# Optimization experiments

Hardware: AMD Instinct MI355X
Metric: run time of the kernel (lower is better)

Reference implementation:

```python
import jax, jax.numpy as jnp
from jax import lax
import numpy as np

B, C, H, W, K = 8, 256, 128, 128, 4


def setup_inputs() -> dict:
    key = jax.random.key(0)
    ks = jax.random.split(key, 21)
    s = 0.05
    return {
        'frm_feat': jax.random.normal(ks[0], (B, C, H, W), jnp.float32),
        'other_feat': jax.random.normal(ks[1], (B, C, H, W), jnp.float32),
        'conv3x3_w': jax.random.normal(ks[2], (C, 2 * C, 3, 3), jnp.float32) * (1.0 / np.sqrt(2 * C * 9).astype(np.float32)),
        'conv3x3_b': jax.random.normal(ks[3], (C,), jnp.float32) * s,
        'a1_w': jax.random.normal(ks[4], (C, 2), jnp.float32) * s,
        'a1_b': jax.random.normal(ks[5], (C,), jnp.float32) * s,
        'a2_w': jax.random.normal(ks[6], (C, 2), jnp.float32) * s,
        'a2_b': jax.random.normal(ks[7], (C,), jnp.float32) * s,
        'a3_w': jax.random.normal(ks[8], (C, 2), jnp.float32) * s,
        'a3_b': jax.random.normal(ks[9], (C,), jnp.float32) * s,
        'ug_w': jax.random.normal(ks[10], (K, C), jnp.float32) * (1.0 / np.sqrt(C).astype(np.float32)),
        'ug_b': jax.random.normal(ks[11], (K,), jnp.float32) * s,
        'recon_w': jax.random.normal(ks[12], (C, C), jnp.float32) * (1.0 / np.sqrt(C).astype(np.float32)),
        'recon_b': jax.random.normal(ks[13], (C,), jnp.float32) * s,
        'sp_w': jax.random.normal(ks[14], (), jnp.float32),
        'sp_b': jax.random.normal(ks[15], (), jnp.float32) * s,
        'spa_w': jax.random.normal(ks[16], (C, C), jnp.float32) * (1.0 / np.sqrt(C).astype(np.float32)),
        'spa_b': jax.random.normal(ks[17], (C,), jnp.float32) * s,
        'spm_w': jax.random.normal(ks[18], (C, C), jnp.float32) * (1.0 / np.sqrt(C).astype(np.float32)),
        'spm_b': jax.random.normal(ks[19], (C,), jnp.float32) * s,
        'alpha': jnp.float32(0.5),
    }


def _make_U(mode, aw, ab, ug_w, ug_b):
    # mode: [B, N, M] -> U: [B, N, K] (softmax over rank K)
    avg = jnp.mean(mode, axis=2)           # [B, N]
    mx = jnp.max(mode, axis=2)             # [B, N]
    feat = jnp.stack([avg, mx], axis=1)    # [B, 2, N]
    feat = jnp.einsum('co,bon->bcn', aw, feat) + ab[None, :, None]  # adapter 1x1 conv: [B, C, N]
    logits = jnp.einsum('kc,bcn->bnk', ug_w, feat) + ug_b           # U_gen 1x1 conv: [B, N, K]
    return jax.nn.softmax(logits, axis=-1)


def reference(frm_feat, other_feat, conv3x3_w, conv3x3_b, a1_w, a1_b, a2_w, a2_b,
              a3_w, a3_b, ug_w, ug_b, recon_w, recon_b, sp_w, sp_b,
              spa_w, spa_b, spm_w, spm_b, alpha):
    b, c, h, w = frm_feat.shape
    x = jnp.concatenate([frm_feat, other_feat], axis=1)  # [B, 2C, H, W]
    Fm = lax.conv_general_dilated(x, conv3x3_w, (1, 1), 'SAME',
                                  dimension_numbers=('NCHW', 'OIHW', 'NCHW'))
    Fm = Fm + conv3x3_b[None, :, None, None]
    Fm = jnp.where(Fm >= 0, Fm, 0.01 * Fm)  # LeakyReLU(0.01)

    # Three mode unfoldings (same math as torch permute/reshape chains)
    mode1 = Fm.reshape(b, c, h * w)                     # [B, C, HW]
    mode2 = jnp.transpose(Fm, (0, 3, 1, 2)).reshape(b, w, c * h)  # [B, W, CH]
    mode3 = jnp.transpose(Fm, (0, 2, 1, 3)).reshape(b, h, c * w)  # [B, H, CW]

    U1 = _make_U(mode1, a1_w, a1_b, ug_w, ug_b)  # [B, C, K]
    U2 = _make_U(mode2, a2_w, a2_b, ug_w, ug_b)  # [B, W, K]
    U3 = _make_U(mode3, a3_w, a3_b, ug_w, ug_b)  # [B, H, K]

    # CP outer-product reconstruction summed over rank, already in [B,C,H,W] layout
    cp = jnp.einsum('bck,bwk,bhk->bchw', U1, U2, U3)
    cp = jnp.einsum('oc,bchw->bohw', recon_w, cp) + recon_b[None, :, None, None]

    # spatial attention: sigmoid(1x1 conv on U3 @ U2^T)
    spatial_att = jax.nn.sigmoid(sp_w * jnp.einsum('bhk,bwk->bhw', U3, U2)[:, None] + sp_b)  # [B,1,H,W]

    # spectral attention
    U23 = jnp.concatenate([U2, U3], axis=1)              # [B, W+H, K]
    F_spe = jnp.einsum('bck,bnk->bcn', U1, U23)          # [B, C, W+H]
    g_avg = jnp.mean(F_spe, axis=-1)                     # [B, C]
    g_max = jnp.max(F_spe, axis=-1)                      # [B, C]
    spec = jax.nn.sigmoid(g_avg @ spa_w.T + spa_b + g_max @ spm_w.T + spm_b)
    spec = jax.nn.sigmoid(spec)[:, :, None, None]        # double sigmoid as in source, [B,C,1,1]

    Watt = spec * spatial_att                            # [B, C, H, W]
    fused = alpha * Watt * frm_feat + (1.0 - alpha) * (1.0 - Watt) * other_feat
    return fused, cp
```

## Files before the change

### kernel.cpp

```cpp
#include <hip/hip_runtime.h>
#include <math.h>

#define BB 8
#define CC 256
#define HH 128
#define WW 128
#define CP_OFF 33554432

#define ZB_OFF   0
#define P1S_OFF  256
#define P1M_OFF  262400
#define P2S_OFF  524544
#define P2M_OFF  525568
#define P3S_OFF  526592
#define P3M_OFF  527616
#define U2_OFF   528640
#define U3_OFF   532736
#define V1_OFF   536832
#define SPEC_OFF 545024
#define WS_ZERO_BYTES (528640 * 4)

typedef __attribute__((ext_vector_type(8))) short bf16x8;
typedef __attribute__((ext_vector_type(4))) float f32x4;

static __device__ __forceinline__ unsigned short f2bf(float f) {
    unsigned u = __float_as_uint(f);
    unsigned r = u + 0x7FFFu + ((u >> 16) & 1u);
    return (unsigned short)(r >> 16);
}
static __device__ __forceinline__ unsigned fkey(float f) {
    unsigned u = __float_as_uint(f);
    return (u & 0x80000000u) ? ~u : (u | 0x80000000u);
}
static __device__ __forceinline__ float fkeydec(unsigned k) {
    return __uint_as_float((k & 0x80000000u) ? (k & 0x7FFFFFFFu) : ~k);
}
static __device__ __forceinline__ void gl_lds16(const void* g, void* l) {
    typedef const __attribute__((address_space(1))) unsigned int* gas_t;
    typedef __attribute__((address_space(3))) unsigned int* las_t;
    gas_t gp = (gas_t)(uintptr_t)g;
    las_t lp = (las_t)(unsigned int)(uintptr_t)l;
    __builtin_amdgcn_global_load_lds(gp, lp, 16, 0, 0);
}

__global__ __launch_bounds__(256) void wt_kernel(
    const float* __restrict__ cw, unsigned short* __restrict__ WtF)
{
    const int g = blockIdx.x * 256 + threadIdx.x;
    const int co = g >> 9, ci = g & 511;
    const int fg = co >> 4, l15c = co & 15;
    const int cic = ci >> 5, l4c = (ci >> 3) & 3, e = ci & 7;
    const int lane = l4c * 16 + l15c;
    const float* s = cw + (size_t)g * 9;
    #pragma unroll
    for (int kh = 0; kh < 3; kh++)
        #pragma unroll
        for (int kw = 0; kw < 3; kw++) {
            const size_t dst =
                ((((size_t)(kh * 16 + cic) * 3 + kw) * 16 + fg) * 64 + lane) * 8 + e;
            WtF[dst] = f2bf(s[kh * 3 + kw]);
        }
}

__global__ __launch_bounds__(256) void xt_kernel(
    const float* __restrict__ frm, const float* __restrict__ oth,
    unsigned short* __restrict__ Xt)
{
    const int w = threadIdx.x & 127, half = threadIdx.x >> 7;
    const int h = blockIdx.x, b = blockIdx.y;
    const float* src = half ? oth : frm;
    const size_t inbase = (((size_t)b * 256) << 14) + ((size_t)h << 7) + w;
    unsigned short* op = Xt + ((((size_t)(b * 128 + h) * 128) + w) << 9) + half * 256;
    #pragma unroll 2
    for (int c8 = 0; c8 < 32; c8++) {
        unsigned short u[8];
        #pragma unroll
        for (int j = 0; j < 8; j++)
            u[j] = f2bf(src[inbase + (((size_t)(c8 * 8 + j)) << 14)]);
        uint4 pk;
        pk.x = (unsigned)u[0] | ((unsigned)u[1] << 16);
        pk.y = (unsigned)u[2] | ((unsigned)u[3] << 16);
        pk.z = (unsigned)u[4] | ((unsigned)u[5] << 16);
        pk.w = (unsigned)u[6] | ((unsigned)u[7] << 16);
        *(uint4*)(op + c8 * 8) = pk;
    }
}

__global__ __launch_bounds__(256, 2) void conv_mfma(
    const unsigned short* __restrict__ WtF,
    const unsigned short* __restrict__ Xt,
    const float* __restrict__ cb,
    const unsigned short* __restrict__ zb,
    float* __restrict__ p1s, unsigned* __restrict__ p1m,
    float* __restrict__ p2s, unsigned* __restrict__ p2m,
    float* __restrict__ p3s, unsigned* __restrict__ p3m)
{
    __shared__ __align__(16) unsigned short lB[2][544 * 8];

    const int tid = threadIdx.x;
    const int swz = (blockIdx.x & 7) * 256 + (blockIdx.x >> 3);
    const int b = swz >> 8;
    const int h = (swz >> 1) & 127;
    const int cohalf = swz & 1;

    const int lane = tid & 63, wid = tid >> 6;
    const int wm = wid & 1, wn = wid >> 1;
    const int l15 = lane & 15, l4 = lane >> 4;
    const int fgBase = cohalf * 8 + wm * 4;

    const unsigned short* baseB[3];
    bool okB[3];
    int dstB[3];
    #pragma unroll
    for (int j = 0; j < 3; j++) {
        const int wi = j * 64 + lane;
        const int wg = wi - 1;
        okB[j] = (wg >= 0) && (wg < WW);
        baseB[j] = Xt + (size_t)b * 8388608
                      + (size_t)(okB[j] ? wg : 0) * 512 + wid * 8;
        dstB[j] = (wid * 136 + j * 64) * 8;
    }
    const unsigned short* baseA = WtF + (size_t)fgBase * 512 + (size_t)lane * 8;

    f32x4 acc[4][4];
    #pragma unroll
    for (int m = 0; m < 4; m++)
        #pragma unroll
        for (int n = 0; n < 4; n++)
            acc[m][n] = (f32x4){0.f, 0.f, 0.f, 0.f};

    auto stageB = [&](int q, int bufi) {
        const int kh = q >> 4;
        const int ci0 = (q & 15) << 5;
        const int hr = h + kh - 1;
        const bool hv = (hr >= 0) && (hr < HH);
        const int boff = (hv ? hr : 0) * 65536 + ci0;
        #pragma unroll
        for (int j = 0; j < 2; j++) {
            const unsigned short* s = (hv && okB[j]) ? (baseB[j] + boff) : zb;
            gl_lds16(s, &lB[bufi][dstB[j]]);
        }
        {
            const unsigned short* s = (hv && okB[2]) ? (baseB[2] + boff) : zb;
            if (lane < 8) gl_lds16(s, &lB[bufi][dstB[2]]);
        }
    };

    auto loadA = [&](int q, bf16x8 (&r)[12]) {
        const unsigned short* p = baseA + (size_t)q * 24576;
        #pragma unroll
        for (int kw = 0; kw < 3; kw++)
            #pragma unroll
            for (int m = 0; m < 4; m++)
                r[kw * 4 + m] = *(const bf16x8*)(p + kw * 8192 + m * 512);
    };

    auto compute = [&](const unsigned short* Bl, bf16x8 (&rA)[12]) {
        #pragma unroll
        for (int kw = 0; kw < 3; kw++) {
            bf16x8 bfr[4];
            #pragma unroll
            for (int n = 0; n < 4; n++) {
                const int unit = l4 * 136 + wn * 64 + n * 16 + l15 + kw;
                bfr[n] = *(const bf16x8*)&Bl[unit * 8];
            }
            #pragma unroll
            for (int m = 0; m < 4; m++)
                #pragma unroll
                for (int n = 0; n < 4; n++)
                    acc[m][n] = __builtin_amdgcn_mfma_f32_16x16x32_bf16(
                        rA[kw * 4 + m], bfr[n], acc[m][n], 0, 0, 0);
        }
    };

    bf16x8 rA0[12], rA1[12];

    stageB(0, 0);
    loadA(0, rA0);

    #pragma unroll 1
    for (int q = 0; q < 46; q += 2) {
        stageB(q + 1, 1);
        loadA(q + 1, rA1);
        __builtin_amdgcn_sched_barrier(0);
        asm volatile("s_waitcnt vmcnt(15)" ::: "memory");
        __builtin_amdgcn_s_barrier();
        __builtin_amdgcn_sched_barrier(0);
        __builtin_amdgcn_s_setprio(1);
        compute(lB[0], rA0);
        __builtin_amdgcn_s_setprio(0);
        __builtin_amdgcn_sched_barrier(0);
        __builtin_amdgcn_s_barrier();

        stageB(q + 2, 0);
        loadA(q + 2, rA0);
        __builtin_amdgcn_sched_barrier(0);
        asm volatile("s_waitcnt vmcnt(15)" ::: "memory");
        __builtin_amdgcn_s_barrier();
        __builtin_amdgcn_sched_barrier(0);
        __builtin_amdgcn_s_setprio(1);
        compute(lB[1], rA1);
        __builtin_amdgcn_s_setprio(0);
        __builtin_amdgcn_sched_barrier(0);
        __builtin_amdgcn_s_barrier();
    }
    stageB(47, 1);
    loadA(47, rA1);
    __builtin_amdgcn_sched_barrier(0);
    asm volatile("s_waitcnt vmcnt(15)" ::: "memory");
    __builtin_amdgcn_s_barrier();
    __builtin_amdgcn_sched_barrier(0);
    __builtin_amdgcn_s_setprio(1);
    compute(lB[0], rA0);
    __builtin_amdgcn_s_setprio(0);
    __builtin_amdgcn_sched_barrier(0);
    asm volatile("s_waitcnt vmcnt(0)" ::: "memory");
    __builtin_amdgcn_s_barrier();
    __builtin_amdgcn_s_setprio(1);
    compute(lB[1], rA1);
    __builtin_amdgcn_s_setprio(0);

    const int cob = cohalf * 128 + wm * 64;
    float t1s[4][4], t1m[4][4], s2[4], x2[4];
    #pragma unroll
    for (int n = 0; n < 4; n++) { s2[n] = 0.f; x2[n] = -INFINITY; }

    #pragma unroll
    for (int m = 0; m < 4; m++) {
        const float4 bb4 = *(const float4*)&cb[cob + m * 16 + l4 * 4];
        float bbv[4] = { bb4.x, bb4.y, bb4.z, bb4.w };
        #pragma unroll
        for (int r = 0; r < 4; r++) { t1s[m][r] = 0.f; t1m[m][r] = -INFINITY; }
        #pragma unroll
        for (int n = 0; n < 4; n++) {
            #pragma unroll
            for (int r = 0; r < 4; r++) {
                float v = acc[m][n][r] + bbv[r];
                v = (v >= 0.f) ? v : 0.01f * v;
                t1s[m][r] += v;
                t1m[m][r] = fmaxf(t1m[m][r], v);
                s2[n] += v;
                x2[n] = fmaxf(x2[n], v);
            }
        }
    }
    #pragma unroll
    for (int m = 0; m < 4; m++)
        #pragma unroll
        for (int r = 0; r < 4; r++) {
            float s = t1s[m][r], x = t1m[m][r];
            #pragma unroll
            for (int off = 1; off <= 8; off <<= 1) {
                s += __shfl_xor(s, off);
                x = fmaxf(x, __shfl_xor(x, off));
            }
            t1s[m][r] = s; t1m[m][r] = x;
        }
    if (l15 == 0) {
        #pragma unroll
        for (int m = 0; m < 4; m++)
            #pragma unroll
            for (int r = 0; r < 4; r++) {
                const int co = cob + m * 16 + l4 * 4 + r;
                const int idx = (b * 256 + co) * 128 + h;
                atomicAdd(&p1s[idx], t1s[m][r]);
                atomicMax(&p1m[idx], fkey(t1m[m][r]));
            }
    }
    float s3 = 0.f, x3 = -INFINITY;
    #pragma unroll
    for (int n = 0; n < 4; n++) {
        float s = s2[n], x = x2[n];
        s += __shfl_xor(s, 16); s += __shfl_xor(s, 32);
        x = fmaxf(x, __shfl_xor(x, 16)); x = fmaxf(x, __shfl_xor(x, 32));
        if (l4 == n) {
            const int w = wn * 64 + n * 16 + l15;
            atomicAdd(&p2s[b * 128 + w], s);
            atomicMax(&p2m[b * 128 + w], fkey(x));
        }
        s3 += s; x3 = fmaxf(x3, x);
    }
    #pragma unroll
    for (int off = 1; off <= 8; off <<= 1) {
        s3 += __shfl_xor(s3, off);
        x3 = fmaxf(x3, __shfl_xor(x3, off));
    }
    if (lane == 0) {
        atomicAdd(&p3s[b * 128 + h], s3);
        atomicMax(&p3m[b * 128 + h], fkey(x3));
    }
}

__device__ inline float blockSum256(float v, float* red)
{
    #pragma unroll
    for (int off = 32; off >= 1; off >>= 1) v += __shfl_xor(v, off);
    const int wave = threadIdx.x >> 6, lane = threadIdx.x & 63;
    __syncthreads();
    if (lane == 0) red[wave] = v;
    __syncthreads();
    return red[0] + red[1] + red[2] + red[3];
}

__device__ inline void softmax4(const float* A, const float* M, const float* Bc,
                                float avg, float mx, float* u)
{
    float l0 = fmaf(A[0], avg, fmaf(M[0], mx, Bc[0]));
    float l1 = fmaf(A[1], avg, fmaf(M[1], mx, Bc[1]));
    float l2 = fmaf(A[2], avg, fmaf(M[2], mx, Bc[2]));
    float l3 = fmaf(A[3], avg, fmaf(M[3], mx, Bc[3]));
    const float mm = fmaxf(fmaxf(l0, l1), fmaxf(l2, l3));
    const float e0 = expf(l0 - mm), e1 = expf(l1 - mm);
    const float e2 = expf(l2 - mm), e3 = expf(l3 - mm);
    const float inv = 1.f / (e0 + e1 + e2 + e3);
    u[0] = e0 * inv; u[1] = e1 * inv; u[2] = e2 * inv; u[3] = e3 * inv;
}

__global__ void make_u_kernel(
    const float* __restrict__ p1s, const unsigned* __restrict__ p1m,
    const float* __restrict__ p2s, const unsigned* __restrict__ p2m,
    const float* __restrict__ p3s, const unsigned* __restrict__ p3m,
    const float* __restrict__ a1w, const float* __restrict__ a1b,
    const float* __restrict__ a2w, const float* __restrict__ a2b,
    const float* __restrict__ a3w, const float* __restrict__ a3b,
    const float* __restrict__ ugw, const float* __restrict__ ugb,
    const float* __restrict__ rw,
    const float* __restrict__ spaw, const float* __restrict__ spab,
    const float* __restrict__ spmw, const float* __restrict__ spmb,
    float* __restrict__ U2g, float* __restrict__ U3g,
    float* __restrict__ V1g, float* __restrict__ specg)
{
    const int b = blockIdx.x, tid = threadIdx.x;

    __shared__ float red[4];
    __shared__ float coefA[3][4], coefM[3][4], coefB[3][4];
    __shared__ float U1s[256][4], U2s[128][4], U3s[128][4];
    __shared__ float gavg[256], gmax[256];

    const float* aws[3]  = { a1w, a2w, a3w };
    const float* abs_[3] = { a1b, a2b, a3b };
    for (int m = 0; m < 3; m++) {
        for (int k = 0; k < 4; k++) {
            const float u = ugw[k * 256 + tid];
            float va = u * aws[m][tid * 2 + 0];
            float vm = u * aws[m][tid * 2 + 1];
            float vb = u * abs_[m][tid];
            va = blockSum256(va, red);
            vm = blockSum256(vm, red);
            vb = blockSum256(vb, red);
            if (tid == 0) {
                coefA[m][k] = va; coefM[m][k] = vm; coefB[m][k] = vb + ugb[k];
            }
        }
    }
    __syncthreads();

    {
        const float* ps = p1s + ((size_t)b * 256 + tid) * 128;
        const unsigned* pm = p1m + ((size_t)b * 256 + tid) * 128;
        float s = 0.f, mx = -INFINITY;
        for (int hh = 0; hh < 128; hh++) {
            s += ps[hh];
            mx = fmaxf(mx, fkeydec(pm[hh]));
        }
        float u[4];
        softmax4(coefA[0], coefM[0], coefB[0], s * (1.f / 16384.f), mx, u);
        U1s[tid][0] = u[0]; U1s[tid][1] = u[1]; U1s[tid][2] = u[2]; U1s[tid][3] = u[3];
    }
    if (tid < 128) {
        const float avg = p2s[b * 128 + tid] * (1.f / 32768.f);
        const float mx  = fkeydec(p2m[b * 128 + tid]);
        float u[4];
        softmax4(coefA[1], coefM[1], coefB[1], avg, mx, u);
        float* g = U2g + ((size_t)b * 128 + tid) * 4;
        for (int k = 0; k < 4; k++) { U2s[tid][k] = u[k]; g[k] = u[k]; }
    } else {
        const int hh = tid - 128;
        const float avg = p3s[b * 128 + hh] * (1.f / 32768.f);
        const float mx  = fkeydec(p3m[b * 128 + hh]);
        float u[4];
        softmax4(coefA[2], coefM[2], coefB[2], avg, mx, u);
        float* g = U3g + ((size_t)b * 128 + hh) * 4;
        for (int k = 0; k < 4; k++) { U3s[hh][k] = u[k]; g[k] = u[k]; }
    }
    __syncthreads();

    {
        float v0 = 0.f, v1 = 0.f, v2 = 0.f, v3 = 0.f;
        const float* rrow = rw + (size_t)tid * 256;
        for (int c2 = 0; c2 < 256; c2++) {
            const float r = rrow[c2];
            v0 = fmaf(r, U1s[c2][0], v0);
            v1 = fmaf(r, U1s[c2][1], v1);
            v2 = fmaf(r, U1s[c2][2], v2);
            v3 = fmaf(r, U1s[c2][3], v3);
        }
        float* vp = V1g + ((size_t)b * 256 + tid) * 4;
        vp[0] = v0; vp[1] = v1; vp[2] = v2; vp[3] = v3;
    }
    {
        const float a0 = U1s[tid][0], a1 = U1s[tid][1];
        const float a2 = U1s[tid][2], a3 = U1s[tid][3];
        float s = 0.f, m = -INFINITY;
        for (int n = 0; n < 256; n++) {
            const float* u23 = (n < 128) ? U2s[n] : U3s[n - 128];
            const float val = a0 * u23[0] + a1 * u23[1] + a2 * u23[2] + a3 * u23[3];
            s += val; m = fmaxf(m, val);
        }
        gavg[tid] = s * (1.f / 256.f);
        gmax[tid] = m;
    }
    __syncthreads();
    {
        float s = spab[tid] + spmb[tid];
        const float* wa = spaw + (size_t)tid * 256;
        const float* wmp = spmw + (size_t)tid * 256;
        for (int c2 = 0; c2 < 256; c2++) {
            s = fmaf(gavg[c2], wa[c2], s);
            s = fmaf(gmax[c2], wmp[c2], s);
        }
        float sg = 1.f / (1.f + expf(-s));
        sg = 1.f / (1.f + expf(-sg));
        specg[b * 256 + tid] = sg;
    }
}

__global__ __launch_bounds__(256) void final_kernel(
    const float* __restrict__ frm, const float* __restrict__ oth,
    const float* __restrict__ U2g, const float* __restrict__ U3g,
    const float* __restrict__ V1g, const float* __restrict__ specg,
    const float* __restrict__ rb,  const float* __restrict__ spw,
    const float* __restrict__ spb, const float* __restrict__ alphap,
    float* __restrict__ out)
{
    const int w  = threadIdx.x & 127;
    const int cc = threadIdx.x >> 7;
    const int h  = blockIdx.x;
    const int c  = blockIdx.y * 2 + cc;
    const int b  = blockIdx.z;

    const float4 u2 = *(const float4*)(U2g + ((size_t)b * 128 + w) * 4);
    const float4 u3 = *(const float4*)(U3g + ((size_t)b * 128 + h) * 4);
    const float4 v1 = *(const float4*)(V1g + ((size_t)b * 256 + c) * 4);

    const float p0 = u2.x * u3.x, p1 = u2.y * u3.y;
    const float p2 = u2.z * u3.z, p3 = u2.w * u3.w;
    const float dot = p0 + p1 + p2 + p3;
    const float att = 1.f / (1.f + expf(-(spw[0] * dot + spb[0])));
    const float cp  = v1.x * p0 + v1.y * p1 + v1.z * p2 + v1.w * p3 + rb[c];

    const float spec  = specg[b * 256 + c];
    const float Watt  = spec * att;
    const float alpha = alphap[0];

    const size_t idx = (((size_t)b * 256 + c) << 14) + ((size_t)h << 7) + w;
    const float f = frm[idx], o = oth[idx];
    out[idx]          = alpha * Watt * f + (1.f - alpha) * (1.f - Watt) * o;
    out[CP_OFF + idx] = cp;
}

extern "C" void kernel_launch(void* const* d_in, const int* in_sizes, int n_in,
                              void* d_out, int out_size, void* d_ws, size_t ws_size,
                              hipStream_t stream)
{
    const float* frm   = (const float*)d_in[0];
    const float* oth   = (const float*)d_in[1];
    const float* cw    = (const float*)d_in[2];
    const float* cb    = (const float*)d_in[3];
    const float* a1w   = (const float*)d_in[4];
    const float* a1b   = (const float*)d_in[5];
    const float* a2w   = (const float*)d_in[6];
    const float* a2b   = (const float*)d_in[7];
    const float* a3w   = (const float*)d_in[8];
    const float* a3b   = (const float*)d_in[9];
    const float* ugw   = (const float*)d_in[10];
    const float* ugb   = (const float*)d_in[11];
    const float* rw    = (const float*)d_in[12];
    const float* rb    = (const float*)d_in[13];
    const float* spw   = (const float*)d_in[14];
    const float* spb   = (const float*)d_in[15];
    const float* spaw  = (const float*)d_in[16];
    const float* spab  = (const float*)d_in[17];
    const float* spmw  = (const float*)d_in[18];
    const float* spmb  = (const float*)d_in[19];
    const float* alpha = (const float*)d_in[20];

    float* out = (float*)d_out;
    float* ws  = (float*)d_ws;

    unsigned short* Wt = (unsigned short*)out;
    unsigned short* Xt = (unsigned short*)(out + CP_OFF);

    float*    zb  = ws + ZB_OFF;
    float*    p1s = ws + P1S_OFF;
    unsigned* p1m = (unsigned*)(ws + P1M_OFF);
    float*    p2s = ws + P2S_OFF;
    unsigned* p2m = (unsigned*)(ws + P2M_OFF);
    float*    p3s = ws + P3S_OFF;
    unsigned* p3m = (unsigned*)(ws + P3M_OFF);
    float*    U2g = ws + U2_OFF;
    float*    U3g = ws + U3_OFF;
    float*    V1g = ws + V1_OFF;
    float*    spc = ws + SPEC_OFF;

    hipMemsetAsync(d_ws, 0, WS_ZERO_BYTES, stream);

    wt_kernel<<<dim3(512), 256, 0, stream>>>(cw, Wt);
    xt_kernel<<<dim3(HH, BB), 256, 0, stream>>>(frm, oth, Xt);

    conv_mfma<<<dim3(2048), 256, 0, stream>>>(
        Wt, Xt, cb, (const unsigned short*)zb,
        p1s, p1m, p2s, p2m, p3s, p3m);

    make_u_kernel<<<dim3(BB), 256, 0, stream>>>(
        p1s, p1m, p2s, p2m, p3s, p3m,
        a1w, a1b, a2w, a2b, a3w, a3b, ugw, ugb,
        rw, spaw, spab, spmw, spmb,
        U2g, U3g, V1g, spc);

    final_kernel<<<dim3(HH, CC / 2, BB), 256, 0, stream>>>(
        frm, oth, U2g, U3g, V1g, spc, rb, spw, spb, alpha, out);
}
```

Baseline: 1.018 ms.

## Enlarge conv tile to two rows, single-buffer A, and split make_u into parallel kernels

The 3x3 conv kernel now has each block compute two output rows (with a double-sized LDS B buffer and 8 N-tiles per wave), halving the grid. A fragments are loaded once per step into a single register set instead of being double-buffered. Per-row p1 stats are written directly rather than atomically, and p2 atomics are rearranged. The serial make_u kernel is split into a coefficient kernel, a parallel U kernel over (batch, part), and a post kernel that computes V1 across many blocks, raising parallelism in the tail stages. The trade-offs are higher register and LDS pressure in the conv kernel, which may reduce occupancy, and less overlap of A loads with compute.

```diff
diff --git a/kernel.cpp b/kernel.cpp
--- a/kernel.cpp
+++ b/kernel.cpp
@@ -20,6 +20,9 @@
 #define SPEC_OFF 545024
 #define WS_ZERO_BYTES (528640 * 4)
 
+#define U1G_OUT_OFF 16777216
+#define CF_OUT_OFF  16785408
+
 typedef __attribute__((ext_vector_type(8))) short bf16x8;
 typedef __attribute__((ext_vector_type(4))) float f32x4;
 
@@ -95,135 +98,125 @@
     float* __restrict__ p2s, unsigned* __restrict__ p2m,
     float* __restrict__ p3s, unsigned* __restrict__ p3m)
 {
-    __shared__ __align__(16) unsigned short lB[2][544 * 8];
+    __shared__ __align__(16) unsigned short lB[2][1088 * 8];
 
     const int tid = threadIdx.x;
-    const int swz = (blockIdx.x & 7) * 256 + (blockIdx.x >> 3);
-    const int b = swz >> 8;
-    const int h = (swz >> 1) & 127;
+    const int swz = (blockIdx.x & 7) * 128 + (blockIdx.x >> 3);
+    const int b = swz >> 7;
+    const int h0 = (swz >> 1) & 63;
     const int cohalf = swz & 1;
 
     const int lane = tid & 63, wid = tid >> 6;
-    const int wm = wid & 1, wn = wid >> 1;
+    const int wm = wid & 1, row = wid >> 1;
     const int l15 = lane & 15, l4 = lane >> 4;
+    const int hout = h0 * 2 + row;
     const int fgBase = cohalf * 8 + wm * 4;
 
-    const unsigned short* baseB[3];
-    bool okB[3];
-    int dstB[3];
-    #pragma unroll
-    for (int j = 0; j < 3; j++) {
-        const int wi = j * 64 + lane;
+    const int rB = wid >> 1;
+    const unsigned short* baseB[5];
+    bool okB[5];
+    #pragma unroll
+    for (int j = 0; j < 5; j++) {
+        const int u = wid * 272 + ((j < 4) ? j * 64 : 256) + lane;
+        const int rem = u - rB * 544;
+        const int ku = ((unsigned)rem) / 136u;
+        const int wi = rem - ku * 136;
         const int wg = wi - 1;
-        okB[j] = (wg >= 0) && (wg < WW);
+        okB[j] = ((unsigned)wg) < 128u;
         baseB[j] = Xt + (size_t)b * 8388608
-                      + (size_t)(okB[j] ? wg : 0) * 512 + wid * 8;
-        dstB[j] = (wid * 136 + j * 64) * 8;
+                      + (size_t)(okB[j] ? wg : 0) * 512 + ku * 8;
     }
     const unsigned short* baseA = WtF + (size_t)fgBase * 512 + (size_t)lane * 8;
 
-    f32x4 acc[4][4];
+    f32x4 acc[4][8];
     #pragma unroll
     for (int m = 0; m < 4; m++)
         #pragma unroll
-        for (int n = 0; n < 4; n++)
+        for (int n = 0; n < 8; n++)
             acc[m][n] = (f32x4){0.f, 0.f, 0.f, 0.f};
+
+    bf16x8 rA[12];
 
     auto stageB = [&](int q, int bufi) {
         const int kh = q >> 4;
         const int ci0 = (q & 15) << 5;
-        const int hr = h + kh - 1;
+        const int hr = h0 * 2 + rB + kh - 1;
         const bool hv = (hr >= 0) && (hr < HH);
         const int boff = (hv ? hr : 0) * 65536 + ci0;
         #pragma unroll
-        for (int j = 0; j < 2; j++) {
+        for (int j = 0; j < 4; j++) {
             const unsigned short* s = (hv && okB[j]) ? (baseB[j] + boff) : zb;
-            gl_lds16(s, &lB[bufi][dstB[j]]);
+            gl_lds16(s, &lB[bufi][(wid * 272 + j * 64) * 8]);
         }
         {
-            const unsigned short* s = (hv && okB[2]) ? (baseB[2] + boff) : zb;
-            if (lane < 8) gl_lds16(s, &lB[bufi][dstB[2]]);
+            const unsigned short* s = (hv && okB[4]) ? (baseB[4] + boff) : zb;
+            if (lane < 16) gl_lds16(s, &lB[bufi][(wid * 272 + 256) * 8]);
         }
     };
 
-    auto loadA = [&](int q, bf16x8 (&r)[12]) {
+    auto loadA = [&](int q) {
         const unsigned short* p = baseA + (size_t)q * 24576;
         #pragma unroll
         for (int kw = 0; kw < 3; kw++)
             #pragma unroll
             for (int m = 0; m < 4; m++)
-                r[kw * 4 + m] = *(const bf16x8*)(p + kw * 8192 + m * 512);
+                rA[kw * 4 + m] = *(const bf16x8*)(p + kw * 8192 + m * 512);
     };
 
-    auto compute = [&](const unsigned short* Bl, bf16x8 (&rA)[12]) {
+    auto compute = [&](int cur) {
+        const unsigned short* Bl = lB[cur];
         #pragma unroll
         for (int kw = 0; kw < 3; kw++) {
-            bf16x8 bfr[4];
-            #pragma unroll
-            for (int n = 0; n < 4; n++) {
-                const int unit = l4 * 136 + wn * 64 + n * 16 + l15 + kw;
-                bfr[n] = *(const bf16x8*)&Bl[unit * 8];
-            }
-            #pragma unroll
-            for (int m = 0; m < 4; m++)
+            #pragma unroll
+            for (int nh = 0; nh < 2; nh++) {
+                bf16x8 bfr[4];
                 #pragma unroll
-                for (int n = 0; n < 4; n++)
-                    acc[m][n] = __builtin_amdgcn_mfma_f32_16x16x32_bf16(
-                        rA[kw * 4 + m], bfr[n], acc[m][n], 0, 0, 0);
+                for (int nn = 0; nn < 4; nn++) {
+                    const int unit = row * 544 + l4 * 136
+                                   + (nh * 4 + nn) * 16 + l15 + kw;
+                    bfr[nn] = *(const bf16x8*)&Bl[unit * 8];
+                }
+                #pragma unroll
+                for (int m = 0; m < 4; m++)
+                    #pragma unroll
+                    for (int nn = 0; nn < 4; nn++)
+                        acc[m][nh * 4 + nn] = __builtin_amdgcn_mfma_f32_16x16x32_bf16(
+                            rA[kw * 4 + m], bfr[nn], acc[m][nh * 4 + nn], 0, 0, 0);
+            }
         }
     };
 
-    bf16x8 rA0[12], rA1[12];
-
     stageB(0, 0);
-    loadA(0, rA0);
+    loadA(0);
 
     #pragma unroll 1
-    for (int q = 0; q < 46; q += 2) {
-        stageB(q + 1, 1);
-        loadA(q + 1, rA1);
+    for (int q = 0; q < 47; q++) {
+        const int cur = q & 1;
+        stageB(q + 1, cur ^ 1);
         __builtin_amdgcn_sched_barrier(0);
-        asm volatile("s_waitcnt vmcnt(15)" ::: "memory");
+        asm volatile("s_waitcnt vmcnt(5)" ::: "memory");
+        __builtin_amdgcn_sched_barrier(0);
         __builtin_amdgcn_s_barrier();
         __builtin_amdgcn_sched_barrier(0);
         __builtin_amdgcn_s_setprio(1);
-        compute(lB[0], rA0);
+        compute(cur);
         __builtin_amdgcn_s_setprio(0);
+        loadA(q + 1);
         __builtin_amdgcn_sched_barrier(0);
         __builtin_amdgcn_s_barrier();
-
-        stageB(q + 2, 0);
-        loadA(q + 2, rA0);
-        __builtin_amdgcn_sched_barrier(0);
-        asm volatile("s_waitcnt vmcnt(15)" ::: "memory");
-        __builtin_amdgcn_s_barrier();
-        __builtin_amdgcn_sched_barrier(0);
-        __builtin_amdgcn_s_setprio(1);
-        compute(lB[1], rA1);
-        __builtin_amdgcn_s_setprio(0);
-        __builtin_amdgcn_sched_barrier(0);
-        __builtin_amdgcn_s_barrier();
-    }
-    stageB(47, 1);
-    loadA(47, rA1);
+    }
+    asm volatile("s_waitcnt vmcnt(0)" ::: "memory");
     __builtin_amdgcn_sched_barrier(0);
-    asm volatile("s_waitcnt vmcnt(15)" ::: "memory");
     __builtin_amdgcn_s_barrier();
     __builtin_amdgcn_sched_barrier(0);
     __builtin_amdgcn_s_setprio(1);
-    compute(lB[0], rA0);
+    compute(1);
     __builtin_amdgcn_s_setprio(0);
-    __builtin_amdgcn_sched_barrier(0);
-    asm volatile("s_waitcnt vmcnt(0)" ::: "memory");
-    __builtin_amdgcn_s_barrier();
-    __builtin_amdgcn_s_setprio(1);
-    compute(lB[1], rA1);
-    __builtin_amdgcn_s_setprio(0);
 
     const int cob = cohalf * 128 + wm * 64;
-    float t1s[4][4], t1m[4][4], s2[4], x2[4];
-    #pragma unroll
-    for (int n = 0; n < 4; n++) { s2[n] = 0.f; x2[n] = -INFINITY; }
+    float t1s[4][4], t1m[4][4], s2[8], x2[8];
+    #pragma unroll
+    for (int n = 0; n < 8; n++) { s2[n] = 0.f; x2[n] = -INFINITY; }
 
     #pragma unroll
     for (int m = 0; m < 4; m++) {
@@ -232,7 +225,7 @@
         #pragma unroll
         for (int r = 0; r < 4; r++) { t1s[m][r] = 0.f; t1m[m][r] = -INFINITY; }
         #pragma unroll
-        for (int n = 0; n < 4; n++) {
+        for (int n = 0; n < 8; n++) {
             #pragma unroll
             for (int r = 0; r < 4; r++) {
                 float v = acc[m][n][r] + bbv[r];
@@ -262,32 +255,38 @@
             #pragma unroll
             for (int r = 0; r < 4; r++) {
                 const int co = cob + m * 16 + l4 * 4 + r;
-                const int idx = (b * 256 + co) * 128 + h;
-                atomicAdd(&p1s[idx], t1s[m][r]);
-                atomicMax(&p1m[idx], fkey(t1m[m][r]));
-            }
+                const int idx = (b * 256 + co) * 128 + hout;
+                p1s[idx] = t1s[m][r];
+                p1m[idx] = fkey(t1m[m][r]);
+            }
+    }
+    #pragma unroll
+    for (int n = 0; n < 8; n++) {
+        s2[n] += __shfl_xor(s2[n], 16); s2[n] += __shfl_xor(s2[n], 32);
+        x2[n] = fmaxf(x2[n], __shfl_xor(x2[n], 16));
+        x2[n] = fmaxf(x2[n], __shfl_xor(x2[n], 32));
+    }
+    #pragma unroll
+    for (int base = 0; base < 8; base += 4) {
+        float sv = s2[base + 0], xv = x2[base + 0];
+        if (l4 == 1) { sv = s2[base + 1]; xv = x2[base + 1]; }
+        if (l4 == 2) { sv = s2[base + 2]; xv = x2[base + 2]; }
+        if (l4 == 3) { sv = s2[base + 3]; xv = x2[base + 3]; }
+        const int w = base * 16 + lane;
+        atomicAdd(&p2s[b * 128 + w], sv);
+        atomicMax(&p2m[b * 128 + w], fkey(xv));
     }
     float s3 = 0.f, x3 = -INFINITY;
     #pragma unroll
-    for (int n = 0; n < 4; n++) {
-        float s = s2[n], x = x2[n];
-        s += __shfl_xor(s, 16); s += __shfl_xor(s, 32);
-        x = fmaxf(x, __shfl_xor(x, 16)); x = fmaxf(x, __shfl_xor(x, 32));
-        if (l4 == n) {
-            const int w = wn * 64 + n * 16 + l15;
-            atomicAdd(&p2s[b * 128 + w], s);
-            atomicMax(&p2m[b * 128 + w], fkey(x));
-        }
-        s3 += s; x3 = fmaxf(x3, x);
-    }
+    for (int n = 0; n < 8; n++) { s3 += s2[n]; x3 = fmaxf(x3, x2[n]); }
     #pragma unroll
     for (int off = 1; off <= 8; off <<= 1) {
         s3 += __shfl_xor(s3, off);
         x3 = fmaxf(x3, __shfl_xor(x3, off));
     }
     if (lane == 0) {
-        atomicAdd(&p3s[b * 128 + h], s3);
-        atomicMax(&p3m[b * 128 + h], fkey(x3));
+        atomicAdd(&p3s[b * 128 + hout], s3);
+        atomicMax(&p3m[b * 128 + hout], fkey(x3));
     }
 }
 
@@ -302,41 +301,32 @@
     return red[0] + red[1] + red[2] + red[3];
 }
 
-__device__ inline void softmax4(const float* A, const float* M, const float* Bc,
-                                float avg, float mx, float* u)
-{
-    float l0 = fmaf(A[0], avg, fmaf(M[0], mx, Bc[0]));
-    float l1 = fmaf(A[1], avg, fmaf(M[1], mx, Bc[1]));
-    float l2 = fmaf(A[2], avg, fmaf(M[2], mx, Bc[2]));
-    float l3 = fmaf(A[3], avg, fmaf(M[3], mx, Bc[3]));
-    const float mm = fmaxf(fmaxf(l0, l1), fmaxf(l2, l3));
-    const float e0 = expf(l0 - mm), e1 = expf(l1 - mm);
-    const float e2 = expf(l2 - mm), e3 = expf(l3 - mm);
+__device__ inline void softmax4c(const float* cf, int m, float avg, float mx, float* u)
+{
+    float l[4];
+    #pragma unroll
+    for (int k = 0; k < 4; k++) {
+        const float A = cf[(m * 4 + k) * 3 + 0];
+        const float M = cf[(m * 4 + k) * 3 + 1];
+        const float B = cf[(m * 4 + k) * 3 + 2];
+        l[k] = fmaf(A, avg, fmaf(M, mx, B));
+    }
+    const float mm = fmaxf(fmaxf(l[0], l[1]), fmaxf(l[2], l[3]));
+    const float e0 = expf(l[0] - mm), e1 = expf(l[1] - mm);
+    const float e2 = expf(l[2] - mm), e3 = expf(l[3] - mm);
     const float inv = 1.f / (e0 + e1 + e2 + e3);
     u[0] = e0 * inv; u[1] = e1 * inv; u[2] = e2 * inv; u[3] = e3 * inv;
 }
 
-__global__ void make_u_kernel(
-    const float* __restrict__ p1s, const unsigned* __restrict__ p1m,
-    const float* __restrict__ p2s, const unsigned* __restrict__ p2m,
-    const float* __restrict__ p3s, const unsigned* __restrict__ p3m,
+__global__ __launch_bounds__(256) void coef_kernel(
     const float* __restrict__ a1w, const float* __restrict__ a1b,
     const float* __restrict__ a2w, const float* __restrict__ a2b,
     const float* __restrict__ a3w, const float* __restrict__ a3b,
     const float* __restrict__ ugw, const float* __restrict__ ugb,
-    const float* __restrict__ rw,
-    const float* __restrict__ spaw, const float* __restrict__ spab,
-    const float* __restrict__ spmw, const float* __restrict__ spmb,
-    float* __restrict__ U2g, float* __restrict__ U3g,
-    float* __restrict__ V1g, float* __restrict__ specg)
-{
-    const int b = blockIdx.x, tid = threadIdx.x;
-
+    float* __restrict__ cf)
+{
+    const int tid = threadIdx.x;
     __shared__ float red[4];
-    __shared__ float coefA[3][4], coefM[3][4], coefB[3][4];
-    __shared__ float U1s[256][4], U2s[128][4], U3s[128][4];
-    __shared__ float gavg[256], gmax[256];
-
     const float* aws[3]  = { a1w, a2w, a3w };
     const float* abs_[3] = { a1b, a2b, a3b };
     for (int m = 0; m < 3; m++) {
@@ -349,79 +339,137 @@
             vm = blockSum256(vm, red);
             vb = blockSum256(vb, red);
             if (tid == 0) {
-                coefA[m][k] = va; coefM[m][k] = vm; coefB[m][k] = vb + ugb[k];
-            }
-        }
-    }
-    __syncthreads();
-
-    {
-        const float* ps = p1s + ((size_t)b * 256 + tid) * 128;
-        const unsigned* pm = p1m + ((size_t)b * 256 + tid) * 128;
+                cf[(m * 4 + k) * 3 + 0] = va;
+                cf[(m * 4 + k) * 3 + 1] = vm;
+                cf[(m * 4 + k) * 3 + 2] = vb + ugb[k];
+            }
+        }
+    }
+}
+
+__global__ __launch_bounds__(256) void u_kernel(
+    const float* __restrict__ p1s, const unsigned* __restrict__ p1m,
+    const float* __restrict__ p2s, const unsigned* __restrict__ p2m,
+    const float* __restrict__ p3s, const unsigned* __restrict__ p3m,
+    const float* __restrict__ cf,
+    float* __restrict__ U1g, float* __restrict__ U2g, float* __restrict__ U3g)
+{
+    const int b = blockIdx.x, y = blockIdx.y, tid = threadIdx.x;
+    if (y < 4) {
+        const int c = y * 64 + (tid >> 2);
+        const int seg = tid & 3;
+        const float* ps = p1s + ((size_t)b * 256 + c) * 128 + seg * 32;
+        const unsigned* pm = p1m + ((size_t)b * 256 + c) * 128 + seg * 32;
         float s = 0.f, mx = -INFINITY;
-        for (int hh = 0; hh < 128; hh++) {
-            s += ps[hh];
-            mx = fmaxf(mx, fkeydec(pm[hh]));
-        }
-        float u[4];
-        softmax4(coefA[0], coefM[0], coefB[0], s * (1.f / 16384.f), mx, u);
-        U1s[tid][0] = u[0]; U1s[tid][1] = u[1]; U1s[tid][2] = u[2]; U1s[tid][3] = u[3];
-    }
-    if (tid < 128) {
-        const float avg = p2s[b * 128 + tid] * (1.f / 32768.f);
-        const float mx  = fkeydec(p2m[b * 128 + tid]);
-        float u[4];
-        softmax4(coefA[1], coefM[1], coefB[1], avg, mx, u);
-        float* g = U2g + ((size_t)b * 128 + tid) * 4;
-        for (int k = 0; k < 4; k++) { U2s[tid][k] = u[k]; g[k] = u[k]; }
+        #pragma unroll 8
+        for (int i = 0; i < 32; i++) {
+            s += ps[i];
+            mx = fmaxf(mx, fkeydec(pm[i]));
+        }
+        s += __shfl_xor(s, 1); s += __shfl_xor(s, 2);
+        mx = fmaxf(mx, __shfl_xor(mx, 1));
+        mx = fmaxf(mx, __shfl_xor(mx, 2));
+        if (seg == 0) {
+            float u[4];
+            softmax4c(cf, 0, s * (1.f / 16384.f), mx, u);
+            float4* g = (float4*)(U1g + ((size_t)b * 256 + c) * 4);
+            *g = make_float4(u[0], u[1], u[2], u[3]);
+        }
     } else {
-        const int hh = tid - 128;
-        const float avg = p3s[b * 128 + hh] * (1.f / 32768.f);
-        const float mx  = fkeydec(p3m[b * 128 + hh]);
-        float u[4];
-        softmax4(coefA[2], coefM[2], coefB[2], avg, mx, u);
-        float* g = U3g + ((size_t)b * 128 + hh) * 4;
-        for (int k = 0; k < 4; k++) { U3s[hh][k] = u[k]; g[k] = u[k]; }
-    }
-    __syncthreads();
-
-    {
-        float v0 = 0.f, v1 = 0.f, v2 = 0.f, v3 = 0.f;
-        const float* rrow = rw + (size_t)tid * 256;
-        for (int c2 = 0; c2 < 256; c2++) {
-            const float r = rrow[c2];
-            v0 = fmaf(r, U1s[c2][0], v0);
-            v1 = fmaf(r, U1s[c2][1], v1);
-            v2 = fmaf(r, U1s[c2][2], v2);
-            v3 = fmaf(r, U1s[c2][3], v3);
-        }
-        float* vp = V1g + ((size_t)b * 256 + tid) * 4;
-        vp[0] = v0; vp[1] = v1; vp[2] = v2; vp[3] = v3;
-    }
-    {
-        const float a0 = U1s[tid][0], a1 = U1s[tid][1];
-        const float a2 = U1s[tid][2], a3 = U1s[tid][3];
+        if (tid < 128) {
+            const float avg = p2s[b * 128 + tid] * (1.f / 32768.f);
+            const float mx  = fkeydec(p2m[b * 128 + tid]);
+            float u[4];
+            softmax4c(cf, 1, avg, mx, u);
+            float4* g = (float4*)(U2g + ((size_t)b * 128 + tid) * 4);
+            *g = make_float4(u[0], u[1], u[2], u[3]);
+        } else {
+            const int hh = tid - 128;
+            const float avg = p3s[b * 128 + hh] * (1.f / 32768.f);
+            const float mx  = fkeydec(p3m[b * 128 + hh]);
+            float u[4];
+            softmax4c(cf, 2, avg, mx, u);
+            float4* g = (float4*)(U3g + ((size_t)b * 128 + hh) * 4);
+            *g = make_float4(u[0], u[1], u[2], u[3]);
+        }
+    }
+}
+
+__global__ __launch_bounds__(256) void post_kernel(
+    const float* __restrict__ U1g, const float* __restrict__ U2g,
+    const float* __restrict__ U3g, const float* __restrict__ rw,
+    const float* __restrict__ spaw, const float* __restrict__ spab,
+    const float* __restrict__ spmw, const float* __restrict__ spmb,
+    float* __restrict__ V1g, float* __restrict__ specg)
+{
+    const int tid = threadIdx.x;
+    if (blockIdx.x < 8) {
+        const int b = blockIdx.x;
+        __shared__ float4 U1s[256];
+        __shared__ float4 U23[256];
+        __shared__ float gavg[256], gmax[256];
+        U1s[tid] = ((const float4*)U1g)[b * 256 + tid];
+        U23[tid] = (tid < 128) ? ((const float4*)U2g)[b * 128 + tid]
+                               : ((const float4*)U3g)[b * 128 + tid - 128];
+        __syncthreads();
+        const float4 a = U1s[tid];
         float s = 0.f, m = -INFINITY;
         for (int n = 0; n < 256; n++) {
-            const float* u23 = (n < 128) ? U2s[n] : U3s[n - 128];
-            const float val = a0 * u23[0] + a1 * u23[1] + a2 * u23[2] + a3 * u23[3];
+            const float4 u = U23[n];
+            const float val = a.x * u.x + a.y * u.y + a.z * u.z + a.w * u.w;
             s += val; m = fmaxf(m, val);
         }
         gavg[tid] = s * (1.f / 256.f);
         gmax[tid] = m;
-    }
-    __syncthreads();
-    {
-        float s = spab[tid] + spmb[tid];
+        __syncthreads();
+        float acc = spab[tid] + spmb[tid];
         const float* wa = spaw + (size_t)tid * 256;
-        const float* wmp = spmw + (size_t)tid * 256;
+        const float* wm = spmw + (size_t)tid * 256;
         for (int c2 = 0; c2 < 256; c2++) {
-            s = fmaf(gavg[c2], wa[c2], s);
-            s = fmaf(gmax[c2], wmp[c2], s);
-        }
-        float sg = 1.f / (1.f + expf(-s));
+            acc = fmaf(gavg[c2], wa[c2], acc);
+            acc = fmaf(gmax[c2], wm[c2], acc);
+        }
+        float sg = 1.f / (1.f + expf(-acc));
         sg = 1.f / (1.f + expf(-sg));
         specg[b * 256 + tid] = sg;
+    } else {
+        const int och = blockIdx.x - 8;
+        const int o = och * 64 + (tid >> 2);
+        const int seg = tid & 3;
+        __shared__ float4 U1all[2048];
+        for (int i = tid; i < 2048; i += 256)
+            U1all[i] = ((const float4*)U1g)[i];
+        __syncthreads();
+        f32x4 vac[8];
+        #pragma unroll
+        for (int bb = 0; bb < 8; bb++) vac[bb] = (f32x4){0.f, 0.f, 0.f, 0.f};
+        const float* rrow = rw + (size_t)o * 256 + seg * 64;
+        for (int i = 0; i < 64; i++) {
+            const float r = rrow[i];
+            const int c2 = seg * 64 + i;
+            #pragma unroll
+            for (int bb = 0; bb < 8; bb++) {
+                const float4 u = U1all[bb * 256 + c2];
+                vac[bb][0] = fmaf(r, u.x, vac[bb][0]);
+                vac[bb][1] = fmaf(r, u.y, vac[bb][1]);
+                vac[bb][2] = fmaf(r, u.z, vac[bb][2]);
+                vac[bb][3] = fmaf(r, u.w, vac[bb][3]);
+            }
+        }
+        #pragma unroll
+        for (int bb = 0; bb < 8; bb++)
+            #pragma unroll
+            for (int k = 0; k < 4; k++) {
+                vac[bb][k] += __shfl_xor(vac[bb][k], 1);
+                vac[bb][k] += __shfl_xor(vac[bb][k], 2);
+            }
+        if (seg == 0) {
+            #pragma unroll
+            for (int bb = 0; bb < 8; bb++) {
+                float4* vp = (float4*)(V1g + ((size_t)bb * 256 + o) * 4);
+                *vp = make_float4(vac[bb][0], vac[bb][1], vac[bb][2], vac[bb][3]);
+            }
+        }
     }
 }
 
@@ -490,6 +538,8 @@
 
     unsigned short* Wt = (unsigned short*)out;
     unsigned short* Xt = (unsigned short*)(out + CP_OFF);
+    float* U1g = out + U1G_OUT_OFF;
+    float* cf  = out + CF_OUT_OFF;
 
     float*    zb  = ws + ZB_OFF;
     float*    p1s = ws + P1S_OFF;
@@ -507,16 +557,18 @@
 
     wt_kernel<<<dim3(512), 256, 0, stream>>>(cw, Wt);
     xt_kernel<<<dim3(HH, BB), 256, 0, stream>>>(frm, oth, Xt);
-
-    conv_mfma<<<dim3(2048), 256, 0, stream>>>(
+    coef_kernel<<<dim3(1), 256, 0, stream>>>(
+        a1w, a1b, a2w, a2b, a3w, a3b, ugw, ugb, cf);
+
+    conv_mfma<<<dim3(1024), 256, 0, stream>>>(
         Wt, Xt, cb, (const unsigned short*)zb,
         p1s, p1m, p2s, p2m, p3s, p3m);
 
-    make_u_kernel<<<dim3(BB), 256, 0, stream>>>(
-        p1s, p1m, p2s, p2m, p3s, p3m,
-        a1w, a1b, a2w, a2b, a3w, a3b, ugw, ugb,
-        rw, spaw, spab, spmw, spmb,
-        U2g, U3g, V1g, spc);
+    u_kernel<<<dim3(BB, 5), 256, 0, stream>>>(
+        p1s, p1m, p2s, p2m, p3s, p3m, cf, U1g, U2g, U3g);
+
+    post_kernel<<<dim3(12), 256, 0, stream>>>(
+        U1g, U2g, U3g, rw, spaw, spab, spmw, spmb, V1g, spc);
 
     final_kernel<<<dim3(HH, CC / 2, BB), 256, 0, stream>>>(
         frm, oth, U2g, U3g, V1g, spc, rb, spw, spb, alpha, out);
```

After: 925.5 us. 1.1x faster.
